# Kernel optimization log

Hardware: AMD Instinct MI355X
Metric: run time of the kernel (lower is better)

## Reference

```python
import jax, jax.numpy as jnp
import numpy as np

N_NODES = 100000
N_EDGES = 1600000
H = 64
EPS_SM = 1e-16
NEG_SLOPE = 0.01  # LeakyReLU default
BN_EPS = 1e-5


def leaky_relu(x):
    return jnp.where(x >= 0, x, NEG_SLOPE * x)


def transformer_conv(x, src, tgt, edge_attr, Wq, bq, Wk, bk, Wv, bv, We, Ws, bs):
    # PyG TransformerConv, heads=1, concat=True, root_weight=True, lin_edge bias=False
    n = x.shape[0]
    q = x @ Wq + bq            # [N,H]
    k = x @ Wk + bk            # [N,H]
    v = x @ Wv + bv            # [N,H]
    e = edge_attr @ We         # [E,H]
    ke = k[src] + e            # [E,H]
    score = jnp.sum(q[tgt] * ke, axis=-1) / jnp.sqrt(jnp.float32(H))  # [E]
    # segment softmax over incoming edges of each target node
    m = jax.ops.segment_max(score, tgt, num_segments=n)
    m = jnp.where(jnp.isfinite(m), m, 0.0)
    p = jnp.exp(score - m[tgt])
    denom = jax.ops.segment_sum(p, tgt, num_segments=n)
    alpha = p / (denom[tgt] + EPS_SM)
    msg = (v[src] + e) * alpha[:, None]                  # [E,H]
    out = jax.ops.segment_sum(msg, tgt, num_segments=n)  # [N,H]
    return out + x @ Ws + bs


def batch_norm(x, gamma, beta):
    mean = jnp.mean(x, axis=0)
    var = jnp.mean((x - mean) ** 2, axis=0)
    return (x - mean) / jnp.sqrt(var + BN_EPS) * gamma + beta


def setup_inputs() -> dict:
    key = jax.random.key(0)
    ks = jax.random.split(key, 24)
    s = 0.05
    d = {
        "x": jax.random.normal(ks[0], (N_NODES, 2), jnp.float32),
        "edge_index": jax.random.randint(ks[1], (2, N_EDGES), 0, N_NODES, jnp.int32),
        "edge_attr": jax.random.normal(ks[2], (N_EDGES, 2), jnp.float32),
        "mask": jax.random.uniform(ks[3], (N_NODES,), jnp.float32),
        # gcn1 (in=2)
        "Wq1": jax.random.normal(ks[4], (2, H)) * s, "bq1": jnp.zeros((H,)),
        "Wk1": jax.random.normal(ks[5], (2, H)) * s, "bk1": jnp.zeros((H,)),
        "Wv1": jax.random.normal(ks[6], (2, H)) * s, "bv1": jnp.zeros((H,)),
        "We1": jax.random.normal(ks[7], (2, H)) * s,
        "Ws1": jax.random.normal(ks[8], (2, H)) * s, "bs1": jnp.zeros((H,)),
        # gcn2 (in=64)
        "Wq2": jax.random.normal(ks[9], (H, H)) * s, "bq2": jnp.zeros((H,)),
        "Wk2": jax.random.normal(ks[10], (H, H)) * s, "bk2": jnp.zeros((H,)),
        "Wv2": jax.random.normal(ks[11], (H, H)) * s, "bv2": jnp.zeros((H,)),
        "We2": jax.random.normal(ks[12], (2, H)) * s,
        "Ws2": jax.random.normal(ks[13], (H, H)) * s, "bs2": jnp.zeros((H,)),
        # batch norm
        "bn_gamma": jnp.ones((H,)), "bn_beta": jnp.zeros((H,)),
        # final MLP 64->32->1
        "Wf1": jax.random.normal(ks[14], (H, 32)) * s, "bf1": jnp.zeros((32,)),
        "Wf2": jax.random.normal(ks[15], (32, 1)) * s, "bf2": jnp.zeros((1,)),
        "iterations": 3,
    }
    return d


def reference(x, edge_index, edge_attr, mask,
              Wq1, bq1, Wk1, bk1, Wv1, bv1, We1, Ws1, bs1,
              Wq2, bq2, Wk2, bk2, Wv2, bv2, We2, Ws2, bs2,
              bn_gamma, bn_beta, Wf1, bf1, Wf2, bf2, iterations):
    src, tgt = edge_index[0], edge_index[1]
    h = transformer_conv(x, src, tgt, edge_attr, Wq1, bq1, Wk1, bk1, Wv1, bv1, We1, Ws1, bs1)
    h = leaky_relu(batch_norm(h, bn_gamma, bn_beta))
    h = leaky_relu(transformer_conv(h, src, tgt, edge_attr, Wq2, bq2, Wk2, bk2, Wv2, bv2, We2, Ws2, bs2))
    for _ in range(iterations - 1):
        h = leaky_relu(transformer_conv(h, src, tgt, edge_attr, Wq2, bq2, Wk2, bk2, Wv2, bv2, We2, Ws2, bs2))
    out = jnp.squeeze(leaky_relu(h @ Wf1 + bf1) @ Wf2 + bf2, axis=-1)  # [N]
    return out * mask
```

## Files before the change

### kernel.cpp

```cpp
#include <hip/hip_runtime.h>
#include <hip/hip_fp16.h>

#define N_NODES 100000
#define N_EDGES 1600000
#define SCAN_B ((N_NODES + 1023) / 1024)
#define BSHIFT 7
#define NB_BKT ((N_NODES + 127) / 128)
#define BCAP 2560

typedef _Float16 half2_t __attribute__((ext_vector_type(2)));
typedef _Float16 half8_t __attribute__((ext_vector_type(8)));
typedef float f32x4 __attribute__((ext_vector_type(4)));

__device__ __forceinline__ float lrelu(float x) { return x >= 0.f ? x : 0.01f * x; }

__global__ void k_count(const int* __restrict__ tgt, int* __restrict__ deg) {
    int i = blockIdx.x * 256 + threadIdx.x;
    atomicAdd(&deg[tgt[i]], 1);
}

__global__ void k_scan1(const int* __restrict__ deg, int* __restrict__ bsum) {
    __shared__ int s[256];
    int t = threadIdx.x;
    int gi = blockIdx.x * 1024 + t * 4;
    int v = 0;
    if (gi < N_NODES) {
        int4 d = *(const int4*)&deg[gi];
        v = d.x + d.y + d.z + d.w;
    }
    s[t] = v;
    __syncthreads();
    for (int d = 128; d > 0; d >>= 1) {
        if (t < d) s[t] += s[t + d];
        __syncthreads();
    }
    if (t == 0) bsum[blockIdx.x] = s[0];
}

__global__ void k_scan2(int* bsum, int* rowptr) {
    if (threadIdx.x == 0) {
        int run = 0;
        for (int b = 0; b < SCAN_B; b++) {
            int v = bsum[b];
            bsum[b] = run;
            run += v;
        }
        rowptr[N_NODES] = run;
    }
}

__global__ void k_scan3(const int* __restrict__ deg, const int* __restrict__ bsum,
                        int* __restrict__ rowptr, int* __restrict__ fill) {
    __shared__ int s[256];
    int t = threadIdx.x;
    int gi = blockIdx.x * 1024 + t * 4;
    int4 d = make_int4(0, 0, 0, 0);
    if (gi < N_NODES) d = *(const int4*)&deg[gi];
    int tsum = d.x + d.y + d.z + d.w;
    s[t] = tsum;
    __syncthreads();
    for (int dd = 1; dd < 256; dd <<= 1) {
        int val = (t >= dd) ? s[t - dd] : 0;
        __syncthreads();
        s[t] += val;
        __syncthreads();
    }
    int texcl = s[t] - tsum + bsum[blockIdx.x];
    if (gi < N_NODES) {
        int4 w;
        w.x = texcl;
        w.y = texcl + d.x;
        w.z = texcl + d.x + d.y;
        w.w = texcl + d.x + d.y + d.z;
        *(int4*)&rowptr[gi] = w;
        *(int4*)&fill[gi] = w;
    }
}

__global__ void k_scatter(const int* __restrict__ src, const int* __restrict__ tgt,
                          const float2* __restrict__ ea,
                          int* __restrict__ fill, int2* __restrict__ csr) {
    int i = blockIdx.x * 256 + threadIdx.x;
    int t = tgt[i];
    float2 e = ea[i];
    int pos = atomicAdd(&fill[t], 1);
    __half2 h2 = __floats2half2_rn(e.x, e.y);
    csr[pos] = make_int2(src[i], *(int*)&h2);
}

__global__ __launch_bounds__(256) void k_bin1(const int* __restrict__ src,
                                              const int* __restrict__ tgt,
                                              const float2* __restrict__ ea,
                                              int* __restrict__ gCur,
                                              int2* __restrict__ bin) {
    __shared__ int hist[NB_BKT];
    __shared__ int cur[NB_BKT];
    int tid = threadIdx.x;
    for (int b = tid; b < NB_BKT; b += 256) hist[b] = 0;
    __syncthreads();
    int base = blockIdx.x * 6400;
#pragma unroll 5
    for (int k = 0; k < 25; k++) {
        int i = base + k * 256 + tid;
        atomicAdd(&hist[tgt[i] >> BSHIFT], 1);
    }
    __syncthreads();
    for (int b = tid; b < NB_BKT; b += 256)
        cur[b] = atomicAdd(&gCur[b], hist[b]);
    __syncthreads();
    for (int k = 0; k < 25; k++) {
        int i = base + k * 256 + tid;
        int t = tgt[i];
        int b = t >> BSHIFT;
        float2 e = ea[i];
        int pos = atomicAdd(&cur[b], 1);
        if (pos < BCAP) {
            __half2 h2 = __floats2half2_rn(e.x, e.y);
            int2 rec;
            rec.x = src[i] | ((t & 127) << 20);
            rec.y = *(int*)&h2;
            bin[(size_t)b * BCAP + pos] = rec;
        }
    }
}

__global__ __launch_bounds__(256) void k_bin2(const int* __restrict__ gCnt,
                                              const int2* __restrict__ bin,
                                              int2* __restrict__ csr,
                                              int* __restrict__ fill) {
    __shared__ int cnt[128];
    int tid = threadIdx.x;
    if (tid < 128) cnt[tid] = 0;
    __syncthreads();
    int b = blockIdx.x;
    int nb = min(gCnt[b], BCAP);
    const int2* myb = &bin[(size_t)b * BCAP];
    for (int i = tid; i < nb; i += 256) {
        int2 rec = myb[i];
        int tloc = (rec.x >> 20) & 127;
        int s = rec.x & 0xFFFFF;
        int pos = atomicAdd(&cnt[tloc], 1);
        if (pos < 64) {
            int node = (b << BSHIFT) + tloc;
            csr[((size_t)node << 6) + pos] = make_int2(s | (rec.x & 0xFFF00000), rec.y);
        }
    }
    __syncthreads();
    if (tid < 128) {
        int node = (b << BSHIFT) + tid;
        if (node < N_NODES) fill[node] = min(cnt[tid], 64);
    }
}

__global__ void k_prep2(const float* __restrict__ Wq, const float* __restrict__ Wk,
                        const float* __restrict__ Ws, const float* __restrict__ We,
                        const float* __restrict__ bk, float* __restrict__ Wcomb) {
    int idx = blockIdx.x * 256 + threadIdx.x;
    if (idx >= 9216) return;
    int j = idx / 144;
    int m = idx - j * 144;
    float v = 0.f;
    if (m < 64) {
        float s = 0.f;
        for (int ch = 0; ch < 64; ch++) s += Wq[j * 64 + ch] * Wk[m * 64 + ch];
        v = 0.125f * s;
    } else if (m < 128) {
        v = Ws[j * 64 + (m - 64)];
    } else if (m == 128) {
        float s = 0.f;
        for (int ch = 0; ch < 64; ch++) s += Wq[j * 64 + ch] * bk[ch];
        v = 0.125f * s;
    } else if (m <= 130) {
        float s = 0.f;
        for (int ch = 0; ch < 64; ch++) s += Wq[j * 64 + ch] * We[(m - 129) * 64 + ch];
        v = 0.125f * s;
    }
    Wcomb[idx] = v;
}

__global__ void k_prepb(const float* __restrict__ Wk2, const float* __restrict__ We2,
                        const float* __restrict__ bq2, const float* __restrict__ bk2,
                        const float* __restrict__ bs2, const float* __restrict__ Wq1,
                        const float* __restrict__ Wk1, const float* __restrict__ We1,
                        const float* __restrict__ bq1, const float* __restrict__ bk1,
                        float* __restrict__ bcomb) {
    int t = threadIdx.x;
    if (t >= 160) return;
    float v = 0.f;
    if (t < 64) {
        float s = 0.f;
        for (int i = 0; i < 64; i++) s += Wk2[t * 64 + i] * bq2[i];
        v = 0.125f * s;
    } else if (t < 128) {
        v = bs2[t - 64];
    } else if (t == 128) {
        float s = 0.f;
        for (int i = 0; i < 64; i++) s += bq2[i] * bk2[i];
        v = 0.125f * s;
    } else if (t <= 130) {
        float s = 0.f;
        for (int i = 0; i < 64; i++) s += bq2[i] * We2[(t - 129) * 64 + i];
        v = 0.125f * s;
    } else if (t < 144) {
        v = 0.f;
    } else {
        int t2 = t - 144;
        float s = 0.f;
        if (t2 < 4) {
            int j = t2 >> 1, m = t2 & 1;
            for (int ch = 0; ch < 64; ch++) s += Wq1[j * 64 + ch] * Wk1[m * 64 + ch];
        } else if (t2 < 6) {
            int j = t2 - 4;
            for (int ch = 0; ch < 64; ch++) s += Wq1[j * 64 + ch] * bk1[ch];
        } else if (t2 < 8) {
            int m = t2 - 6;
            for (int ch = 0; ch < 64; ch++) s += bq1[ch] * Wk1[m * 64 + ch];
        } else if (t2 == 8) {
            for (int ch = 0; ch < 64; ch++) s += bq1[ch] * bk1[ch];
        } else if (t2 < 13) {
            int j = (t2 - 9) >> 1, d = (t2 - 9) & 1;
            for (int ch = 0; ch < 64; ch++) s += Wq1[j * 64 + ch] * We1[d * 64 + ch];
        } else if (t2 < 15) {
            int d = t2 - 13;
            for (int ch = 0; ch < 64; ch++) s += bq1[ch] * We1[d * 64 + ch];
        }
        v = 0.125f * s;
    }
    bcomb[t] = v;
}

__global__ void k_prepw(const float* __restrict__ Wcomb, __half* __restrict__ wp) {
    int t = blockIdx.x * 256 + threadIdx.x;
    if (t >= 9216) return;
    int e = t & 7;
    int lane = (t >> 3) & 63;
    int kh = (t >> 9) & 1;
    int fm = t >> 10;
    int k = (kh << 5) + ((lane >> 4) << 3) + e;
    int c = fm * 16 + (lane & 15);
    wp[t] = __float2half(Wcomb[k * 144 + c]);
}

__global__ void k_prepv(const float* __restrict__ Wv, __half* __restrict__ wvp) {
    int t = blockIdx.x * 256 + threadIdx.x;
    if (t >= 4096) return;
    int e = t & 7;
    int lane = (t >> 3) & 63;
    int kh = (t >> 9) & 1;
    int fm = t >> 10;
    int k = (kh << 5) + ((lane >> 4) << 3) + e;
    int c = fm * 16 + (lane & 15);
    wvp[t] = __float2half(Wv[k * 64 + c]);
}

__global__ __launch_bounds__(256) void k_agg1(
    const float* __restrict__ x, const int* __restrict__ idx,
    const int2* __restrict__ csr, const float* __restrict__ Wv,
    const float* __restrict__ We, const float* __restrict__ Ws,
    const float* __restrict__ bv, const float* __restrict__ bs,
    const float* __restrict__ prep, __half* __restrict__ oh, int bucket) {
    int node = blockIdx.x * 4 + (threadIdx.x >> 6);
    int lane = threadIdx.x & 63;
    float2 xt = *(const float2*)&x[(size_t)node << 1];
    float a0 = xt.x * prep[0] + xt.y * prep[2] + prep[6];
    float a1 = xt.x * prep[1] + xt.y * prep[3] + prep[7];
    float b1 = xt.x * prep[4] + xt.y * prep[5] + prep[8];
    float g0 = xt.x * prep[9] + xt.y * prep[11] + prep[13];
    float g1 = xt.x * prep[10] + xt.y * prep[12] + prep[14];

    float l = 0.f, px0 = 0.f, px1 = 0.f, pA = 0.f, pB = 0.f;
    if (bucket) {
        int deg = idx[node];
        bool valid = lane < deg;
        int2 rec = valid ? csr[((size_t)node << 6) + lane] : make_int2(0, 0);
        int src = rec.x & 0xFFFFF;
        float2 ef = __half22float2(*(__half2*)&rec.y);
        float2 xs = valid ? *(const float2*)&x[(size_t)src << 1] : make_float2(0.f, 0.f);
        float t = a0 * xs.x + a1 * xs.y + b1 + g0 * ef.x + g1 * ef.y;
        float pp = valid ? __expf(t) : 0.f;
        l = pp;
        px0 = pp * xs.x;
        px1 = pp * xs.y;
        pA = pp * ef.x;
        pB = pp * ef.y;
    } else {
        int beg = idx[node], end = idx[node + 1];
        for (int p = beg + lane; p < end; p += 64) {
            int2 rec = csr[p];
            float2 ef = __half22float2(*(__half2*)&rec.y);
            float2 xs = *(const float2*)&x[(size_t)rec.x << 1];
            float t = a0 * xs.x + a1 * xs.y + b1 + g0 * ef.x + g1 * ef.y;
            float pp = __expf(t);
            l += pp;
            px0 += pp * xs.x;
            px1 += pp * xs.y;
            pA += pp * ef.x;
            pB += pp * ef.y;
        }
    }
#pragma unroll
    for (int D = 1; D < 64; D <<= 1) {
        l += __shfl_xor(l, D, 64);
        px0 += __shfl_xor(px0, D, 64);
        px1 += __shfl_xor(px1, D, 64);
        pA += __shfl_xor(pA, D, 64);
        pB += __shfl_xor(pB, D, 64);
    }
    float inv = 1.f / (l + 1e-16f);
    int c = lane;
    float r = (px0 * Wv[c] + px1 * Wv[64 + c] + pA * We[c] + pB * We[64 + c] +
               l * bv[c]) * inv +
              xt.x * Ws[c] + xt.y * Ws[64 + c] + bs[c];
    oh[((size_t)node << 6) + c] = __float2half(r);
}

__global__ void k_bnp(const __half* __restrict__ oh, float* __restrict__ bnsum,
                      float* __restrict__ bnsq) {
    __shared__ float s1[256], s2[256];
    int t = threadIdx.x;
    int c = t & 63, nsub = t >> 6;
    float su = 0.f, sq = 0.f;
    int base = blockIdx.x * 400;
    for (int i = 0; i < 100; i++) {
        int node = base + i * 4 + nsub;
        float v = __half2float(oh[((size_t)node << 6) + c]);
        su += v;
        sq += v * v;
    }
    s1[t] = su;
    s2[t] = sq;
    __syncthreads();
    if (t < 64) {
        float a = s1[t] + s1[t + 64] + s1[t + 128] + s1[t + 192];
        float b = s2[t] + s2[t + 64] + s2[t + 128] + s2[t + 192];
        atomicAdd(&bnsum[t], a);
        atomicAdd(&bnsq[t], b);
    }
}

__global__ void k_bnf(const float* bnsum, const float* bnsq, const float* gamma,
                      const float* beta, float* bnab) {
    int c = threadIdx.x;
    float mean = bnsum[c] * (1.f / N_NODES);
    float var = bnsq[c] * (1.f / N_NODES) - mean * mean;
    float A = gamma[c] * rsqrtf(var + 1e-5f);
    bnab[c] = A;
    bnab[64 + c] = beta[c] - mean * A;
}

__global__ void k_bna(const __half* __restrict__ oh, const float* __restrict__ bnab,
                      __half* __restrict__ hh) {
    int idx = blockIdx.x * 256 + threadIdx.x;
    int c = idx & 63;
    float v = lrelu(__half2float(oh[idx]) * bnab[c] + bnab[64 + c]);
    hh[idx] = __float2half(v);
}

__global__ __launch_bounds__(256) void k_gemm(
    const __half* __restrict__ oh, const __half* __restrict__ hhin,
    const __half* __restrict__ wp, const float* __restrict__ bcomb,
    const float* __restrict__ bnab, int use_bn,
    __half* __restrict__ qh, float* __restrict__ ext, __half* __restrict__ hhout) {
    __shared__ __half qsm[64 * 68];
    int tid = threadIdx.x;
    int w = tid >> 6;
    int lane = tid & 63;
    int nloc = lane & 15;
    int kg = lane >> 4;
    int base = blockIdx.x * 64;

    half8_t A[2], AE[2];
    const half8_t* wpv = (const half8_t*)wp;
#pragma unroll
    for (int kh = 0; kh < 2; kh++) A[kh] = wpv[((w << 1) + kh) * 64 + lane];
    if (w == 3) {
#pragma unroll
        for (int kh = 0; kh < 2; kh++) AE[kh] = wpv[((8 << 1) + kh) * 64 + lane];
    }

    half8_t z8;
#pragma unroll
    for (int i = 0; i < 8; i++) z8[i] = (_Float16)0.f;

    half8_t B[4][2];
    int n[4];
    bool g[4];
#pragma unroll
    for (int nf = 0; nf < 4; nf++) {
        n[nf] = base + (nf << 4) + nloc;
        g[nf] = n[nf] < N_NODES;
    }

    if (use_bn) {
        float4 bnA[2][2], bnB[2][2];
#pragma unroll
        for (int kh = 0; kh < 2; kh++) {
            int k0 = (kh << 5) + (kg << 3);
            bnA[kh][0] = *(const float4*)&bnab[k0];
            bnA[kh][1] = *(const float4*)&bnab[k0 + 4];
            bnB[kh][0] = *(const float4*)&bnab[64 + k0];
            bnB[kh][1] = *(const float4*)&bnab[64 + k0 + 4];
        }
        const int4 zi4 = make_int4(0, 0, 0, 0);
#pragma unroll
        for (int nf = 0; nf < 4; nf++) {
            const __half* orow = oh + ((size_t)n[nf] << 6);
#pragma unroll
            for (int kh = 0; kh < 2; kh++) {
                int k0 = (kh << 5) + (kg << 3);
                int4 raw = g[nf] ? *(const int4*)&orow[k0] : zi4;
                const __half2* op = (const __half2*)&raw;
                float2 o01 = __half22float2(op[0]);
                float2 o23 = __half22float2(op[1]);
                float2 o45 = __half22float2(op[2]);
                float2 o67 = __half22float2(op[3]);
                float4 lo, hi;
                lo.x = lrelu(o01.x * bnA[kh][0].x + bnB[kh][0].x);
                lo.y = lrelu(o01.y * bnA[kh][0].y + bnB[kh][0].y);
                lo.z = lrelu(o23.x * bnA[kh][0].z + bnB[kh][0].z);
                lo.w = lrelu(o23.y * bnA[kh][0].w + bnB[kh][0].w);
                hi.x = lrelu(o45.x * bnA[kh][1].x + bnB[kh][1].x);
                hi.y = lrelu(o45.y * bnA[kh][1].y + bnB[kh][1].y);
                hi.z = lrelu(o67.x * bnA[kh][1].z + bnB[kh][1].z);
                hi.w = lrelu(o67.y * bnA[kh][1].w + bnB[kh][1].w);
                half8_t r;
                r[0] = (_Float16)lo.x; r[1] = (_Float16)lo.y;
                r[2] = (_Float16)lo.z; r[3] = (_Float16)lo.w;
                r[4] = (_Float16)hi.x; r[5] = (_Float16)hi.y;
                r[6] = (_Float16)hi.z; r[7] = (_Float16)hi.w;
                B[nf][kh] = r;
                if (g[nf]) *(half8_t*)&hhout[((size_t)n[nf] << 6) + k0] = r;
            }
        }
    } else {
#pragma unroll
        for (int nf = 0; nf < 4; nf++) {
#pragma unroll
            for (int kh = 0; kh < 2; kh++) {
                int k0 = (kh << 5) + (kg << 3);
                B[nf][kh] = g[nf] ? *(const half8_t*)&hhin[((size_t)n[nf] << 6) + k0]
                                  : z8;
            }
        }
    }

    f32x4 acc[4], accE[4];
#pragma unroll
    for (int nf = 0; nf < 4; nf++) {
        acc[nf] = (f32x4){0.f, 0.f, 0.f, 0.f};
        accE[nf] = (f32x4){0.f, 0.f, 0.f, 0.f};
    }

#pragma unroll
    for (int nf = 0; nf < 4; nf++) {
        acc[nf] = __builtin_amdgcn_mfma_f32_16x16x32_f16(A[0], B[nf][0], acc[nf],
                                                          0, 0, 0);
        acc[nf] = __builtin_amdgcn_mfma_f32_16x16x32_f16(A[1], B[nf][1], acc[nf],
                                                          0, 0, 0);
    }
    if (w == 3) {
#pragma unroll
        for (int nf = 0; nf < 4; nf++) {
            accE[nf] = __builtin_amdgcn_mfma_f32_16x16x32_f16(AE[0], B[nf][0],
                                                              accE[nf], 0, 0, 0);
            accE[nf] = __builtin_amdgcn_mfma_f32_16x16x32_f16(AE[1], B[nf][1],
                                                              accE[nf], 0, 0, 0);
        }
    }

    int rowg = kg << 2;
    int c0 = (w << 4) + rowg;
    float4 bi = *(const float4*)&bcomb[c0];
#pragma unroll
    for (int nf = 0; nf < 4; nf++) {
        int nl = (nf << 4) + nloc;
        __half2 p0 = __floats2half2_rn(acc[nf][0] + bi.x, acc[nf][1] + bi.y);
        __half2 p1 = __floats2half2_rn(acc[nf][2] + bi.z, acc[nf][3] + bi.w);
        *(__half2*)&qsm[nl * 68 + c0] = p0;
        *(__half2*)&qsm[nl * 68 + c0 + 2] = p1;
    }
    if (w == 3 && kg == 0) {
        float4 be = *(const float4*)&bcomb[128];
#pragma unroll
        for (int nf = 0; nf < 4; nf++) {
            if (!g[nf]) continue;
            float4 r;
            r.x = accE[nf][0] + be.x;
            r.y = accE[nf][1] + be.y;
            r.z = accE[nf][2] + be.z;
            r.w = accE[nf][3] + be.w;
            *(float4*)&ext[(size_t)n[nf] << 2] = r;
        }
    }
    __syncthreads();
#pragma unroll
    for (int rep = 0; rep < 8; rep++) {
        int i = rep * 256 + tid;
        int row = i >> 5;
        int col = (i & 31) << 1;
        if (base + row < N_NODES) {
            int v = *(int*)&qsm[row * 68 + col];
            *(int*)&qh[((size_t)(base + row) << 6) + col] = v;
        }
    }
}

template <int LAST>
__global__ __launch_bounds__(256) void k_fused(
    __half* qh, float* ext,
    const __half* __restrict__ hh_in, __half* __restrict__ hh_out,
    const int* __restrict__ idx, const int2* __restrict__ csr,
    const __half* __restrict__ wp, const __half* __restrict__ wvp,
    const float* __restrict__ We, const float* __restrict__ bv,
    const float* __restrict__ bcomb,
    const float* __restrict__ Wf1, const float* __restrict__ bf1,
    const float* __restrict__ Wf2, const float* __restrict__ bf2v,
    const float* __restrict__ mask, float* __restrict__ out,
    int bucket) {
    constexpr int RSM_BYTES = LAST ? (64 * 68 * 4) : (64 * 72 * 2);
    __shared__ __align__(16) char smem[RSM_BYTES + 9216 + 1024];
    __half* rsm16 = (__half*)smem;
    float* rsm32 = (float*)smem;
    __half* Shatsm = (__half*)(smem + RSM_BYTES);
    __half* qsm = (__half*)(smem + RSM_BYTES);
    float* W1sm = (float*)(smem + RSM_BYTES);
    float4* svecsm = (float4*)(smem + RSM_BYTES + 9216);

    int tid = threadIdx.x;
    int wv = tid >> 6;
    int lane = tid & 63;
    int base = blockIdx.x * 64;

    {
        int es = lane >> 2, cl = lane & 3;
        int jf = ((es & 1) << 3) | ((es & 2) << 1) | ((es & 4) >> 1) | ((es & 8) >> 3);
        int shatcol = (cl << 4) + jf;
        for (int nl = 0; nl < 16; nl++) {
            int node = base + (wv << 4) + nl;
            if (node >= N_NODES) continue;
            float4 ex = *(const float4*)&ext[(size_t)node << 2];
            float beta = ex.x, qe0 = ex.y, qe1 = ex.z;
            int4 qr0 = *(const int4*)&qh[((size_t)node << 6) + (cl << 4)];
            int4 qr1 = *(const int4*)&qh[((size_t)node << 6) + (cl << 4) + 8];
            const half2_t* qp0 = (const half2_t*)&qr0;
            const half2_t* qp1 = (const half2_t*)&qr1;

            float l = 0.f, sA = 0.f, sB = 0.f;
            float accv[16];
#pragma unroll
            for (int c = 0; c < 16; c++) accv[c] = 0.f;

            int nEdge, rbase2;
            if (bucket) {
                nEdge = idx[node];
                rbase2 = node << 6;
            } else {
                rbase2 = idx[node];
                nEdge = idx[node + 1] - rbase2;
            }
            int nIter = (nEdge + 15) >> 4;

            auto body = [&](int4 h0, int4 h1, int2 rec, bool ok) {
                const half2_t* hp0 = (const half2_t*)&h0;
                const half2_t* hp1 = (const half2_t*)&h1;
                float t = 0.f;
#if __has_builtin(__builtin_amdgcn_fdot2)
#pragma unroll
                for (int p = 0; p < 4; p++)
                    t = __builtin_amdgcn_fdot2(hp0[p], qp0[p], t, false);
#pragma unroll
                for (int p = 0; p < 4; p++)
                    t = __builtin_amdgcn_fdot2(hp1[p], qp1[p], t, false);
#else
                const __half* hq0 = (const __half*)&qr0;
                const __half* hq1 = (const __half*)&qr1;
                const __half* hh0 = (const __half*)&h0;
                const __half* hh1 = (const __half*)&h1;
#pragma unroll
                for (int c = 0; c < 8; c++)
                    t += __half2float(hh0[c]) * __half2float(hq0[c]);
#pragma unroll
                for (int c = 0; c < 8; c++)
                    t += __half2float(hh1[c]) * __half2float(hq1[c]);
#endif
                t += __shfl_xor(t, 1, 64);
                t += __shfl_xor(t, 2, 64);
                float2 ef = __half22float2(*(__half2*)&rec.y);
                t += beta + ef.x * qe0 + ef.y * qe1;
                float pp = ok ? __expf(t) : 0.f;
                l += pp;
                sA += pp * ef.x;
                sB += pp * ef.y;
                const __half* hs0 = (const __half*)&h0;
                const __half* hs1 = (const __half*)&h1;
#pragma unroll
                for (int c = 0; c < 8; c++) accv[c] += pp * __half2float(hs0[c]);
#pragma unroll
                for (int c = 0; c < 8; c++) accv[8 + c] += pp * __half2float(hs1[c]);
            };

            if (bucket) {
                int2 recs[4];
#pragma unroll
                for (int i = 0; i < 4; i++) {
                    int e = (i << 4) + es;
                    recs[i] = (e < nEdge) ? csr[(size_t)rbase2 + e] : make_int2(0, 0);
                }
                if (nIter > 0) {
                    int src0 = recs[0].x & 0xFFFFF;
                    const __half* hr = hh_in + ((size_t)src0 << 6) + (cl << 4);
                    int4 h0c = *(const int4*)&hr[0];
                    int4 h1c = *(const int4*)&hr[8];
#pragma unroll
                    for (int i = 0; i < 4; i++) {
                        if (i < nIter) {
                            int4 h0 = h0c, h1 = h1c;
                            if (i + 1 < nIter) {
                                int srcn = recs[i + 1].x & 0xFFFFF;
                                const __half* hrn =
                                    hh_in + ((size_t)srcn << 6) + (cl << 4);
                                h0c = *(const int4*)&hrn[0];
                                h1c = *(const int4*)&hrn[8];
                            }
                            body(h0, h1, recs[i], ((i << 4) + es) < nEdge);
                        }
                    }
                }
            } else {
                for (int i = 0; i < nIter; i++) {
                    int e = (i << 4) + es;
                    bool ok = e < nEdge;
                    int2 rec = ok ? csr[(size_t)rbase2 + e] : make_int2(0, 0);
                    int src = rec.x & 0xFFFFF;
                    const __half* hr = hh_in + ((size_t)src << 6) + (cl << 4);
                    int4 h0 = *(const int4*)&hr[0];
                    int4 h1 = *(const int4*)&hr[8];
                    body(h0, h1, rec, ok);
                }
            }

#pragma unroll
            for (int D = 4; D < 64; D <<= 1) {
                l += __shfl_xor(l, D, 64);
                sA += __shfl_xor(sA, D, 64);
                sB += __shfl_xor(sB, D, 64);
            }
            float inv = 1.f / (l + 1e-16f);

#pragma unroll
            for (int step = 0; step < 4; step++) {
                int m = 4 << step;
                int half = 8 >> step;
                bool up = (lane & m) != 0;
#pragma unroll
                for (int i = 0; i < half; i++) {
                    float send = up ? accv[i] : accv[i + half];
                    float recv = __shfl_xor(send, m, 64);
                    float keep = up ? accv[i + half] : accv[i];
                    accv[i] = keep + recv;
                }
            }
            Shatsm[((wv << 4) + nl) * 72 + shatcol] = __float2half(accv[0] * inv);
            if (lane == 0)
                svecsm[(wv << 4) + nl] = make_float4(sA * inv, sB * inv, l * inv, 0.f);
        }
    }
    __syncthreads();

    {
        int nloc = lane & 15, kg = lane >> 4;
        const half8_t* wvv = (const half8_t*)wvp;
        const half8_t* wpv = (const half8_t*)wp;
        half8_t Av0 = wvv[((wv << 1) + 0) * 64 + lane];
        half8_t Av1 = wvv[((wv << 1) + 1) * 64 + lane];
        half8_t As0 = wpv[(((4 + wv) << 1) + 0) * 64 + lane];
        half8_t As1 = wpv[(((4 + wv) << 1) + 1) * 64 + lane];

        int rowg = kg << 2;
        int c0 = (wv << 4) + rowg;
        float4 we0 = *(const float4*)&We[c0];
        float4 we1 = *(const float4*)&We[64 + c0];
        float4 bv4 = *(const float4*)&bv[c0];
        float4 bs4 = *(const float4*)&bcomb[64 + c0];

        half8_t z8;
#pragma unroll
        for (int i = 0; i < 8; i++) z8[i] = (_Float16)0.f;

#pragma unroll
        for (int nf = 0; nf < 4; nf++) {
            int n = base + (nf << 4) + nloc;
            bool g = n < N_NODES;
            int nl2 = (nf << 4) + nloc;
            const __half* srow = &Shatsm[nl2 * 72];
            const __half* hrow = hh_in + ((size_t)n << 6);
            half8_t Bs0 = g ? *(const half8_t*)&srow[kg << 3] : z8;
            half8_t Bs1 = g ? *(const half8_t*)&srow[32 + (kg << 3)] : z8;
            half8_t Bh0 = g ? *(const half8_t*)&hrow[kg << 3] : z8;
            half8_t Bh1 = g ? *(const half8_t*)&hrow[32 + (kg << 3)] : z8;

            f32x4 acc = (f32x4){0.f, 0.f, 0.f, 0.f};
            acc = __builtin_amdgcn_mfma_f32_16x16x32_f16(Av0, Bs0, acc, 0, 0, 0);
            acc = __builtin_amdgcn_mfma_f32_16x16x32_f16(Av1, Bs1, acc, 0, 0, 0);
            acc = __builtin_amdgcn_mfma_f32_16x16x32_f16(As0, Bh0, acc, 0, 0, 0);
            acc = __builtin_amdgcn_mfma_f32_16x16x32_f16(As1, Bh1, acc, 0, 0, 0);

            float4 sv = g ? svecsm[nl2] : make_float4(0.f, 0.f, 0.f, 0.f);
            float4 r;
            r.x = lrelu(acc[0] + sv.x * we0.x + sv.y * we1.x + sv.z * bv4.x + bs4.x);
            r.y = lrelu(acc[1] + sv.x * we0.y + sv.y * we1.y + sv.z * bv4.y + bs4.y);
            r.z = lrelu(acc[2] + sv.x * we0.z + sv.y * we1.z + sv.z * bv4.z + bs4.z);
            r.w = lrelu(acc[3] + sv.x * we0.w + sv.y * we1.w + sv.z * bv4.w + bs4.w);

            if (LAST) {
                *(float4*)&rsm32[nl2 * 68 + c0] = r;
            } else {
                __half2 p0 = __floats2half2_rn(r.x, r.y);
                __half2 p1 = __floats2half2_rn(r.z, r.w);
                *(__half2*)&rsm16[nl2 * 72 + c0] = p0;
                *(__half2*)&rsm16[nl2 * 72 + c0 + 2] = p1;
            }
        }
    }
    __syncthreads();

    if (!LAST) {
        int nloc = lane & 15, kg = lane >> 4;
        const half8_t* wpv = (const half8_t*)wp;
        half8_t A0 = wpv[((wv << 1) + 0) * 64 + lane];
        half8_t A1 = wpv[((wv << 1) + 1) * 64 + lane];
        half8_t AE0 = A0, AE1 = A1;
        if (wv == 3) {
            AE0 = wpv[16 * 64 + lane];
            AE1 = wpv[17 * 64 + lane];
        }
        int rowg = kg << 2;
        int c0 = (wv << 4) + rowg;
        float4 bi = *(const float4*)&bcomb[c0];

#pragma unroll
        for (int nf = 0; nf < 4; nf++) {
            int nl2 = (nf << 4) + nloc;
            const __half* rrow = &rsm16[nl2 * 72];
            half8_t B0 = *(const half8_t*)&rrow[kg << 3];
            half8_t B1 = *(const half8_t*)&rrow[32 + (kg << 3)];
            f32x4 acc = (f32x4){0.f, 0.f, 0.f, 0.f};
            acc = __builtin_amdgcn_mfma_f32_16x16x32_f16(A0, B0, acc, 0, 0, 0);
            acc = __builtin_amdgcn_mfma_f32_16x16x32_f16(A1, B1, acc, 0, 0, 0);
            __half2 p0 = __floats2half2_rn(acc[0] + bi.x, acc[1] + bi.y);
            __half2 p1 = __floats2half2_rn(acc[2] + bi.z, acc[3] + bi.w);
            *(__half2*)&qsm[nl2 * 72 + c0] = p0;
            *(__half2*)&qsm[nl2 * 72 + c0 + 2] = p1;
            if (wv == 3) {
                f32x4 ae = (f32x4){0.f, 0.f, 0.f, 0.f};
                ae = __builtin_amdgcn_mfma_f32_16x16x32_f16(AE0, B0, ae, 0, 0, 0);
                ae = __builtin_amdgcn_mfma_f32_16x16x32_f16(AE1, B1, ae, 0, 0, 0);
                if (kg == 0) {
                    int n = base + nl2;
                    if (n < N_NODES) {
                        float4 be = *(const float4*)&bcomb[128];
                        float4 r;
                        r.x = ae[0] + be.x;
                        r.y = ae[1] + be.y;
                        r.z = ae[2] + be.z;
                        r.w = ae[3] + be.w;
                        *(float4*)&ext[(size_t)n << 2] = r;
                    }
                }
            }
        }
        __syncthreads();
#pragma unroll
        for (int rep = 0; rep < 8; rep++) {
            int i = rep * 256 + tid;
            int row = i >> 5;
            int col = (i & 31) << 1;
            if (base + row < N_NODES) {
                *(int*)&qh[((size_t)(base + row) << 6) + col] =
                    *(int*)&qsm[row * 72 + col];
                *(int*)&hh_out[((size_t)(base + row) << 6) + col] =
                    *(int*)&rsm16[row * 72 + col];
            }
        }
    } else {
        for (int i = tid; i < 2048; i += 256) W1sm[i] = Wf1[i];
        __syncthreads();
        int nl2 = tid >> 2, jg = tid & 3;
        int node = base + nl2;
        float a8[8];
        const float* b1p = &bf1[jg << 3];
#pragma unroll
        for (int k = 0; k < 8; k++) a8[k] = b1p[k];
        const float* hr = &rsm32[nl2 * 68];
        for (int c = 0; c < 64; c++) {
            float hv = hr[c];
            const float* wr = &W1sm[(c << 5) + (jg << 3)];
            float4 wa = *(const float4*)&wr[0];
            float4 wb = *(const float4*)&wr[4];
            a8[0] += hv * wa.x; a8[1] += hv * wa.y;
            a8[2] += hv * wa.z; a8[3] += hv * wa.w;
            a8[4] += hv * wb.x; a8[5] += hv * wb.y;
            a8[6] += hv * wb.z; a8[7] += hv * wb.w;
        }
        const float* w2p = &Wf2[jg << 3];
        float zs = 0.f;
#pragma unroll
        for (int k = 0; k < 8; k++) zs += lrelu(a8[k]) * w2p[k];
        zs += __shfl_xor(zs, 1, 64);
        zs += __shfl_xor(zs, 2, 64);
        if (jg == 0 && node < N_NODES)
            out[node] = (zs + bf2v[0]) * mask[node];
    }
}

extern "C" void kernel_launch(void* const* d_in, const int* in_sizes, int n_in,
                              void* d_out, int out_size, void* d_ws, size_t ws_size,
                              hipStream_t stream) {
    const float* x = (const float*)d_in[0];
    const int* ei = (const int*)d_in[1];
    const float* ea = (const float*)d_in[2];
    const float* mask = (const float*)d_in[3];
    const float *Wq1 = (const float*)d_in[4], *bq1 = (const float*)d_in[5];
    const float *Wk1 = (const float*)d_in[6], *bk1 = (const float*)d_in[7];
    const float *Wv1 = (const float*)d_in[8], *bv1 = (const float*)d_in[9];
    const float *We1 = (const float*)d_in[10];
    const float *Ws1 = (const float*)d_in[11], *bs1 = (const float*)d_in[12];
    const float *Wq2 = (const float*)d_in[13], *bq2 = (const float*)d_in[14];
    const float *Wk2 = (const float*)d_in[15], *bk2 = (const float*)d_in[16];
    const float *Wv2 = (const float*)d_in[17], *bv2 = (const float*)d_in[18];
    const float *We2 = (const float*)d_in[19];
    const float *Ws2 = (const float*)d_in[20], *bs2 = (const float*)d_in[21];
    const float *gamma = (const float*)d_in[22], *beta = (const float*)d_in[23];
    const float *Wf1 = (const float*)d_in[24], *bf1 = (const float*)d_in[25];
    const float *Wf2 = (const float*)d_in[26], *bf2v = (const float*)d_in[27];
    float* out = (float*)d_out;

    const size_t bucket_need =
        (size_t)NB_BKT * BCAP * 8 + (size_t)N_NODES * 64 * 8 +
        (size_t)N_NODES * 64 * 2 * 4 +
        (size_t)N_NODES * 16 +
        (size_t)N_NODES * 4 * 3 + (1 << 20);
    bool use_bucket = ws_size >= bucket_need;

    char* ws = (char*)d_ws;
    size_t off = 0;
    auto alloc = [&](size_t b) {
        size_t r = off;
        off += (b + 255) & ~(size_t)255;
        return r;
    };
    int* deg = (int*)(ws + alloc(N_NODES * 4));
    int* fill = (int*)(ws + alloc(N_NODES * 4));
    int* rowptr = (int*)(ws + alloc((N_NODES + 1) * 4));
    int* bsum = (int*)(ws + alloc(SCAN_B * 4));
    int* gCur = (int*)(ws + alloc(NB_BKT * 4));
    float* bnsum = (float*)(ws + alloc(64 * 4));
    float* bnsq = (float*)(ws + alloc(64 * 4));
    float* bnab = (float*)(ws + alloc(128 * 4));
    float* Wcomb = (float*)(ws + alloc(9216 * 4));
    float* bcomb = (float*)(ws + alloc(160 * 4));
    __half* wp = (__half*)(ws + alloc(9216 * 2));
    __half* wvp = (__half*)(ws + alloc(4096 * 2));
    float* ext = (float*)(ws + alloc((size_t)N_NODES * 16));
    int2* bin1 = (int2*)(ws + alloc(use_bucket ? (size_t)NB_BKT * BCAP * 8 : 256));
    int2* csr = (int2*)(ws + alloc(use_bucket ? (size_t)N_NODES * 64 * 8
                                              : (size_t)N_EDGES * 8));
    __half* qh = (__half*)(ws + alloc((size_t)N_NODES * 64 * 2));
    __half* oh = (__half*)(ws + alloc((size_t)N_NODES * 64 * 2));
    __half* hh0 = (__half*)(ws + alloc((size_t)N_NODES * 64 * 2));
    __half* hh1 = (__half*)(ws + alloc((size_t)N_NODES * 64 * 2));

    const int* srcI = ei;
    const int* tgtI = ei + N_EDGES;

    hipMemsetAsync(bnsum, 0, 64 * 4, stream);
    hipMemsetAsync(bnsq, 0, 64 * 4, stream);

    k_prep2<<<36, 256, 0, stream>>>(Wq2, Wk2, Ws2, We2, bk2, Wcomb);
    k_prepb<<<1, 192, 0, stream>>>(Wk2, We2, bq2, bk2, bs2, Wq1, Wk1, We1, bq1, bk1,
                                   bcomb);
    k_prepw<<<36, 256, 0, stream>>>(Wcomb, wp);
    k_prepv<<<16, 256, 0, stream>>>(Wv2, wvp);

    const int* aggIdx;
    if (use_bucket) {
        hipMemsetAsync(gCur, 0, NB_BKT * 4, stream);
        k_bin1<<<250, 256, 0, stream>>>(srcI, tgtI, (const float2*)ea, gCur, bin1);
        k_bin2<<<NB_BKT, 256, 0, stream>>>(gCur, bin1, csr, fill);
        aggIdx = fill;
    } else {
        hipMemsetAsync(deg, 0, N_NODES * 4, stream);
        k_count<<<N_EDGES / 256, 256, 0, stream>>>(tgtI, deg);
        k_scan1<<<SCAN_B, 256, 0, stream>>>(deg, bsum);
        k_scan2<<<1, 64, 0, stream>>>(bsum, rowptr);
        k_scan3<<<SCAN_B, 256, 0, stream>>>(deg, bsum, rowptr, fill);
        k_scatter<<<N_EDGES / 256, 256, 0, stream>>>(srcI, tgtI, (const float2*)ea,
                                                     fill, csr);
        aggIdx = rowptr;
    }
    int bkt = use_bucket ? 1 : 0;

    k_agg1<<<N_NODES / 4, 256, 0, stream>>>(x, aggIdx, csr, Wv1, We1, Ws1, bv1, bs1,
                                            bcomb + 144, oh, bkt);
    k_bnp<<<250, 256, 0, stream>>>(oh, bnsum, bnsq);
    k_bnf<<<1, 64, 0, stream>>>(bnsum, bnsq, gamma, beta, bnab);
    if (!use_bucket)
        k_bna<<<N_NODES * 64 / 256, 256, 0, stream>>>(oh, bnab, hh0);

    const int gemm_grid = (N_NODES + 63) / 64;
    k_gemm<<<gemm_grid, 256, 0, stream>>>(oh, hh0, wp, bcomb, bnab, bkt, qh, ext,
                                          hh0);
    k_fused<0><<<gemm_grid, 256, 0, stream>>>(qh, ext, hh0, hh1, aggIdx, csr, wp,
                                              wvp, We2, bv2, bcomb, Wf1, bf1, Wf2,
                                              bf2v, mask, out, bkt);
    k_fused<0><<<gemm_grid, 256, 0, stream>>>(qh, ext, hh1, hh0, aggIdx, csr, wp,
                                              wvp, We2, bv2, bcomb, Wf1, bf1, Wf2,
                                              bf2v, mask, out, bkt);
    k_fused<1><<<gemm_grid, 256, 0, stream>>>(qh, ext, hh0, hh1, aggIdx, csr, wp,
                                              wvp, We2, bv2, bcomb, Wf1, bf1, Wf2,
                                              bf2v, mask, out, bkt);
}
```

Before: 531.9 us.

## Fuse BN stats into agg1 and first-layer GEMM into fused conv kernel

BatchNorm partial sums are now computed in k_agg1's epilogue and spread over 32 atomic slots, removing the separate k_bnp pass over the activations. The standalone k_gemm is removed. The first k_fused instance now computes q and the edge-projection terms for its own 64-node tile with MFMA into shared memory, avoiding a global write and re-read of qh and ext. k_bna is now always launched to materialise the normalized activations, which replaces the BN application previously folded into k_gemm. Other blocks' q/ext still come from global memory for later layers, so correctness relies on the later fused kernels reading qh/ext written by this first one.

```diff
diff --git a/kernel.cpp b/kernel.cpp
--- a/kernel.cpp
+++ b/kernel.cpp
@@ -258,9 +258,12 @@
     const int2* __restrict__ csr, const float* __restrict__ Wv,
     const float* __restrict__ We, const float* __restrict__ Ws,
     const float* __restrict__ bv, const float* __restrict__ bs,
-    const float* __restrict__ prep, __half* __restrict__ oh, int bucket) {
-    int node = blockIdx.x * 4 + (threadIdx.x >> 6);
-    int lane = threadIdx.x & 63;
+    const float* __restrict__ prep, __half* __restrict__ oh,
+    float* __restrict__ bnsum, float* __restrict__ bnsq, int bucket) {
+    __shared__ float s1[256], s2[256];
+    int tid = threadIdx.x;
+    int node = blockIdx.x * 4 + (tid >> 6);
+    int lane = tid & 63;
     float2 xt = *(const float2*)&x[(size_t)node << 1];
     float a0 = xt.x * prep[0] + xt.y * prep[2] + prep[6];
     float a1 = xt.x * prep[1] + xt.y * prep[3] + prep[7];
@@ -312,37 +315,28 @@
                l * bv[c]) * inv +
               xt.x * Ws[c] + xt.y * Ws[64 + c] + bs[c];
     oh[((size_t)node << 6) + c] = __float2half(r);
-}
-
-__global__ void k_bnp(const __half* __restrict__ oh, float* __restrict__ bnsum,
-                      float* __restrict__ bnsq) {
-    __shared__ float s1[256], s2[256];
-    int t = threadIdx.x;
-    int c = t & 63, nsub = t >> 6;
-    float su = 0.f, sq = 0.f;
-    int base = blockIdx.x * 400;
-    for (int i = 0; i < 100; i++) {
-        int node = base + i * 4 + nsub;
-        float v = __half2float(oh[((size_t)node << 6) + c]);
-        su += v;
-        sq += v * v;
-    }
-    s1[t] = su;
-    s2[t] = sq;
-    __syncthreads();
-    if (t < 64) {
-        float a = s1[t] + s1[t + 64] + s1[t + 128] + s1[t + 192];
-        float b = s2[t] + s2[t + 64] + s2[t + 128] + s2[t + 192];
-        atomicAdd(&bnsum[t], a);
-        atomicAdd(&bnsq[t], b);
+    s1[tid] = r;
+    s2[tid] = r * r;
+    __syncthreads();
+    if (tid < 64) {
+        float a = s1[tid] + s1[tid + 64] + s1[tid + 128] + s1[tid + 192];
+        float b = s2[tid] + s2[tid + 64] + s2[tid + 128] + s2[tid + 192];
+        int slot = (blockIdx.x & 31) << 6;
+        atomicAdd(&bnsum[slot + tid], a);
+        atomicAdd(&bnsq[slot + tid], b);
     }
 }
 
 __global__ void k_bnf(const float* bnsum, const float* bnsq, const float* gamma,
                       const float* beta, float* bnab) {
     int c = threadIdx.x;
-    float mean = bnsum[c] * (1.f / N_NODES);
-    float var = bnsq[c] * (1.f / N_NODES) - mean * mean;
+    float su = 0.f, sq = 0.f;
+    for (int s = 0; s < 32; s++) {
+        su += bnsum[(s << 6) + c];
+        sq += bnsq[(s << 6) + c];
+    }
+    float mean = su * (1.f / N_NODES);
+    float var = sq * (1.f / N_NODES) - mean * mean;
     float A = gamma[c] * rsqrtf(var + 1e-5f);
     bnab[c] = A;
     bnab[64 + c] = beta[c] - mean * A;
@@ -356,156 +350,7 @@
     hh[idx] = __float2half(v);
 }
 
-__global__ __launch_bounds__(256) void k_gemm(
-    const __half* __restrict__ oh, const __half* __restrict__ hhin,
-    const __half* __restrict__ wp, const float* __restrict__ bcomb,
-    const float* __restrict__ bnab, int use_bn,
-    __half* __restrict__ qh, float* __restrict__ ext, __half* __restrict__ hhout) {
-    __shared__ __half qsm[64 * 68];
-    int tid = threadIdx.x;
-    int w = tid >> 6;
-    int lane = tid & 63;
-    int nloc = lane & 15;
-    int kg = lane >> 4;
-    int base = blockIdx.x * 64;
-
-    half8_t A[2], AE[2];
-    const half8_t* wpv = (const half8_t*)wp;
-#pragma unroll
-    for (int kh = 0; kh < 2; kh++) A[kh] = wpv[((w << 1) + kh) * 64 + lane];
-    if (w == 3) {
-#pragma unroll
-        for (int kh = 0; kh < 2; kh++) AE[kh] = wpv[((8 << 1) + kh) * 64 + lane];
-    }
-
-    half8_t z8;
-#pragma unroll
-    for (int i = 0; i < 8; i++) z8[i] = (_Float16)0.f;
-
-    half8_t B[4][2];
-    int n[4];
-    bool g[4];
-#pragma unroll
-    for (int nf = 0; nf < 4; nf++) {
-        n[nf] = base + (nf << 4) + nloc;
-        g[nf] = n[nf] < N_NODES;
-    }
-
-    if (use_bn) {
-        float4 bnA[2][2], bnB[2][2];
-#pragma unroll
-        for (int kh = 0; kh < 2; kh++) {
-            int k0 = (kh << 5) + (kg << 3);
-            bnA[kh][0] = *(const float4*)&bnab[k0];
-            bnA[kh][1] = *(const float4*)&bnab[k0 + 4];
-            bnB[kh][0] = *(const float4*)&bnab[64 + k0];
-            bnB[kh][1] = *(const float4*)&bnab[64 + k0 + 4];
-        }
-        const int4 zi4 = make_int4(0, 0, 0, 0);
-#pragma unroll
-        for (int nf = 0; nf < 4; nf++) {
-            const __half* orow = oh + ((size_t)n[nf] << 6);
-#pragma unroll
-            for (int kh = 0; kh < 2; kh++) {
-                int k0 = (kh << 5) + (kg << 3);
-                int4 raw = g[nf] ? *(const int4*)&orow[k0] : zi4;
-                const __half2* op = (const __half2*)&raw;
-                float2 o01 = __half22float2(op[0]);
-                float2 o23 = __half22float2(op[1]);
-                float2 o45 = __half22float2(op[2]);
-                float2 o67 = __half22float2(op[3]);
-                float4 lo, hi;
-                lo.x = lrelu(o01.x * bnA[kh][0].x + bnB[kh][0].x);
-                lo.y = lrelu(o01.y * bnA[kh][0].y + bnB[kh][0].y);
-                lo.z = lrelu(o23.x * bnA[kh][0].z + bnB[kh][0].z);
-                lo.w = lrelu(o23.y * bnA[kh][0].w + bnB[kh][0].w);
-                hi.x = lrelu(o45.x * bnA[kh][1].x + bnB[kh][1].x);
-                hi.y = lrelu(o45.y * bnA[kh][1].y + bnB[kh][1].y);
-                hi.z = lrelu(o67.x * bnA[kh][1].z + bnB[kh][1].z);
-                hi.w = lrelu(o67.y * bnA[kh][1].w + bnB[kh][1].w);
-                half8_t r;
-                r[0] = (_Float16)lo.x; r[1] = (_Float16)lo.y;
-                r[2] = (_Float16)lo.z; r[3] = (_Float16)lo.w;
-                r[4] = (_Float16)hi.x; r[5] = (_Float16)hi.y;
-                r[6] = (_Float16)hi.z; r[7] = (_Float16)hi.w;
-                B[nf][kh] = r;
-                if (g[nf]) *(half8_t*)&hhout[((size_t)n[nf] << 6) + k0] = r;
-            }
-        }
-    } else {
-#pragma unroll
-        for (int nf = 0; nf < 4; nf++) {
-#pragma unroll
-            for (int kh = 0; kh < 2; kh++) {
-                int k0 = (kh << 5) + (kg << 3);
-                B[nf][kh] = g[nf] ? *(const half8_t*)&hhin[((size_t)n[nf] << 6) + k0]
-                                  : z8;
-            }
-        }
-    }
-
-    f32x4 acc[4], accE[4];
-#pragma unroll
-    for (int nf = 0; nf < 4; nf++) {
-        acc[nf] = (f32x4){0.f, 0.f, 0.f, 0.f};
-        accE[nf] = (f32x4){0.f, 0.f, 0.f, 0.f};
-    }
-
-#pragma unroll
-    for (int nf = 0; nf < 4; nf++) {
-        acc[nf] = __builtin_amdgcn_mfma_f32_16x16x32_f16(A[0], B[nf][0], acc[nf],
-                                                          0, 0, 0);
-        acc[nf] = __builtin_amdgcn_mfma_f32_16x16x32_f16(A[1], B[nf][1], acc[nf],
-                                                          0, 0, 0);
-    }
-    if (w == 3) {
-#pragma unroll
-        for (int nf = 0; nf < 4; nf++) {
-            accE[nf] = __builtin_amdgcn_mfma_f32_16x16x32_f16(AE[0], B[nf][0],
-                                                              accE[nf], 0, 0, 0);
-            accE[nf] = __builtin_amdgcn_mfma_f32_16x16x32_f16(AE[1], B[nf][1],
-                                                              accE[nf], 0, 0, 0);
-        }
-    }
-
-    int rowg = kg << 2;
-    int c0 = (w << 4) + rowg;
-    float4 bi = *(const float4*)&bcomb[c0];
-#pragma unroll
-    for (int nf = 0; nf < 4; nf++) {
-        int nl = (nf << 4) + nloc;
-        __half2 p0 = __floats2half2_rn(acc[nf][0] + bi.x, acc[nf][1] + bi.y);
-        __half2 p1 = __floats2half2_rn(acc[nf][2] + bi.z, acc[nf][3] + bi.w);
-        *(__half2*)&qsm[nl * 68 + c0] = p0;
-        *(__half2*)&qsm[nl * 68 + c0 + 2] = p1;
-    }
-    if (w == 3 && kg == 0) {
-        float4 be = *(const float4*)&bcomb[128];
-#pragma unroll
-        for (int nf = 0; nf < 4; nf++) {
-            if (!g[nf]) continue;
-            float4 r;
-            r.x = accE[nf][0] + be.x;
-            r.y = accE[nf][1] + be.y;
-            r.z = accE[nf][2] + be.z;
-            r.w = accE[nf][3] + be.w;
-            *(float4*)&ext[(size_t)n[nf] << 2] = r;
-        }
-    }
-    __syncthreads();
-#pragma unroll
-    for (int rep = 0; rep < 8; rep++) {
-        int i = rep * 256 + tid;
-        int row = i >> 5;
-        int col = (i & 31) << 1;
-        if (base + row < N_NODES) {
-            int v = *(int*)&qsm[row * 68 + col];
-            *(int*)&qh[((size_t)(base + row) << 6) + col] = v;
-        }
-    }
-}
-
-template <int LAST>
+template <int FIRST, int LAST>
 __global__ __launch_bounds__(256) void k_fused(
     __half* qh, float* ext,
     const __half* __restrict__ hh_in, __half* __restrict__ hh_out,
@@ -518,18 +363,66 @@
     const float* __restrict__ mask, float* __restrict__ out,
     int bucket) {
     constexpr int RSM_BYTES = LAST ? (64 * 68 * 4) : (64 * 72 * 2);
-    __shared__ __align__(16) char smem[RSM_BYTES + 9216 + 1024];
+    constexpr int EXT_BYTES = FIRST ? 1024 : 0;
+    __shared__ __align__(16) char smem[RSM_BYTES + 9216 + 1024 + EXT_BYTES];
     __half* rsm16 = (__half*)smem;
     float* rsm32 = (float*)smem;
+    __half* qsmA = (__half*)smem;
     __half* Shatsm = (__half*)(smem + RSM_BYTES);
     __half* qsm = (__half*)(smem + RSM_BYTES);
     float* W1sm = (float*)(smem + RSM_BYTES);
     float4* svecsm = (float4*)(smem + RSM_BYTES + 9216);
+    float4* extsm = (float4*)(smem + RSM_BYTES + 9216 + 1024);
 
     int tid = threadIdx.x;
     int wv = tid >> 6;
     int lane = tid & 63;
     int base = blockIdx.x * 64;
+
+    if (FIRST) {
+        int nloc = lane & 15, kg = lane >> 4;
+        const half8_t* wpv = (const half8_t*)wp;
+        half8_t A0 = wpv[((wv << 1) + 0) * 64 + lane];
+        half8_t A1 = wpv[((wv << 1) + 1) * 64 + lane];
+        half8_t AE0 = A0, AE1 = A1;
+        if (wv == 3) {
+            AE0 = wpv[16 * 64 + lane];
+            AE1 = wpv[17 * 64 + lane];
+        }
+        int rowg = kg << 2;
+        int c0 = (wv << 4) + rowg;
+        float4 bi = *(const float4*)&bcomb[c0];
+        half8_t z8;
+#pragma unroll
+        for (int i = 0; i < 8; i++) z8[i] = (_Float16)0.f;
+#pragma unroll
+        for (int nf = 0; nf < 4; nf++) {
+            int n = base + (nf << 4) + nloc;
+            bool g = n < N_NODES;
+            int nl2 = (nf << 4) + nloc;
+            const __half* hrow = hh_in + ((size_t)n << 6);
+            half8_t B0 = g ? *(const half8_t*)&hrow[kg << 3] : z8;
+            half8_t B1 = g ? *(const half8_t*)&hrow[32 + (kg << 3)] : z8;
+            f32x4 acc = (f32x4){0.f, 0.f, 0.f, 0.f};
+            acc = __builtin_amdgcn_mfma_f32_16x16x32_f16(A0, B0, acc, 0, 0, 0);
+            acc = __builtin_amdgcn_mfma_f32_16x16x32_f16(A1, B1, acc, 0, 0, 0);
+            __half2 p0 = __floats2half2_rn(acc[0] + bi.x, acc[1] + bi.y);
+            __half2 p1 = __floats2half2_rn(acc[2] + bi.z, acc[3] + bi.w);
+            *(__half2*)&qsmA[nl2 * 72 + c0] = p0;
+            *(__half2*)&qsmA[nl2 * 72 + c0 + 2] = p1;
+            if (wv == 3) {
+                f32x4 ae = (f32x4){0.f, 0.f, 0.f, 0.f};
+                ae = __builtin_amdgcn_mfma_f32_16x16x32_f16(AE0, B0, ae, 0, 0, 0);
+                ae = __builtin_amdgcn_mfma_f32_16x16x32_f16(AE1, B1, ae, 0, 0, 0);
+                if (kg == 0 && g) {
+                    float4 be = *(const float4*)&bcomb[128];
+                    extsm[nl2] = make_float4(ae[0] + be.x, ae[1] + be.y,
+                                             ae[2] + be.z, ae[3] + be.w);
+                }
+            }
+        }
+        __syncthreads();
+    }
 
     {
         int es = lane >> 2, cl = lane & 3;
@@ -538,10 +431,18 @@
         for (int nl = 0; nl < 16; nl++) {
             int node = base + (wv << 4) + nl;
             if (node >= N_NODES) continue;
-            float4 ex = *(const float4*)&ext[(size_t)node << 2];
+            float4 ex;
+            int4 qr0, qr1;
+            if (FIRST) {
+                ex = extsm[(wv << 4) + nl];
+                qr0 = *(const int4*)&qsmA[((wv << 4) + nl) * 72 + (cl << 4)];
+                qr1 = *(const int4*)&qsmA[((wv << 4) + nl) * 72 + (cl << 4) + 8];
+            } else {
+                ex = *(const float4*)&ext[(size_t)node << 2];
+                qr0 = *(const int4*)&qh[((size_t)node << 6) + (cl << 4)];
+                qr1 = *(const int4*)&qh[((size_t)node << 6) + (cl << 4) + 8];
+            }
             float beta = ex.x, qe0 = ex.y, qe1 = ex.z;
-            int4 qr0 = *(const int4*)&qh[((size_t)node << 6) + (cl << 4)];
-            int4 qr1 = *(const int4*)&qh[((size_t)node << 6) + (cl << 4) + 8];
             const half2_t* qp0 = (const half2_t*)&qr0;
             const half2_t* qp1 = (const half2_t*)&qr1;
 
@@ -854,8 +755,8 @@
     int* rowptr = (int*)(ws + alloc((N_NODES + 1) * 4));
     int* bsum = (int*)(ws + alloc(SCAN_B * 4));
     int* gCur = (int*)(ws + alloc(NB_BKT * 4));
-    float* bnsum = (float*)(ws + alloc(64 * 4));
-    float* bnsq = (float*)(ws + alloc(64 * 4));
+    float* bnsum = (float*)(ws + alloc(32 * 64 * 4));
+    float* bnsq = (float*)(ws + alloc(32 * 64 * 4));
     float* bnab = (float*)(ws + alloc(128 * 4));
     float* Wcomb = (float*)(ws + alloc(9216 * 4));
     float* bcomb = (float*)(ws + alloc(160 * 4));
@@ -873,8 +774,8 @@
     const int* srcI = ei;
     const int* tgtI = ei + N_EDGES;
 
-    hipMemsetAsync(bnsum, 0, 64 * 4, stream);
-    hipMemsetAsync(bnsq, 0, 64 * 4, stream);
+    hipMemsetAsync(bnsum, 0, 32 * 64 * 4, stream);
+    hipMemsetAsync(bnsq, 0, 32 * 64 * 4, stream);
 
     k_prep2<<<36, 256, 0, stream>>>(Wq2, Wk2, Ws2, We2, bk2, Wcomb);
     k_prepb<<<1, 192, 0, stream>>>(Wk2, We2, bq2, bk2, bs2, Wq1, Wk1, We1, bq1, bk1,
@@ -901,22 +802,18 @@
     int bkt = use_bucket ? 1 : 0;
 
     k_agg1<<<N_NODES / 4, 256, 0, stream>>>(x, aggIdx, csr, Wv1, We1, Ws1, bv1, bs1,
-                                            bcomb + 144, oh, bkt);
-    k_bnp<<<250, 256, 0, stream>>>(oh, bnsum, bnsq);
+                                            bcomb + 144, oh, bnsum, bnsq, bkt);
     k_bnf<<<1, 64, 0, stream>>>(bnsum, bnsq, gamma, beta, bnab);
-    if (!use_bucket)
-        k_bna<<<N_NODES * 64 / 256, 256, 0, stream>>>(oh, bnab, hh0);
+    k_bna<<<N_NODES * 64 / 256, 256, 0, stream>>>(oh, bnab, hh0);
 
     const int gemm_grid = (N_NODES + 63) / 64;
-    k_gemm<<<gemm_grid, 256, 0, stream>>>(oh, hh0, wp, bcomb, bnab, bkt, qh, ext,
-                                          hh0);
-    k_fused<0><<<gemm_grid, 256, 0, stream>>>(qh, ext, hh0, hh1, aggIdx, csr, wp,
-                                              wvp, We2, bv2, bcomb, Wf1, bf1, Wf2,
-                                              bf2v, mask, out, bkt);
-    k_fused<0><<<gemm_grid, 256, 0, stream>>>(qh, ext, hh1, hh0, aggIdx, csr, wp,
-                                              wvp, We2, bv2, bcomb, Wf1, bf1, Wf2,
-                                              bf2v, mask, out, bkt);
-    k_fused<1><<<gemm_grid, 256, 0, stream>>>(qh, ext, hh0, hh1, aggIdx, csr, wp,
-                                              wvp, We2, bv2, bcomb, Wf1, bf1, Wf2,
-                                              bf2v, mask, out, bkt);
-}
+    k_fused<1, 0><<<gemm_grid, 256, 0, stream>>>(qh, ext, hh0, hh1, aggIdx, csr, wp,
+                                                 wvp, We2, bv2, bcomb, Wf1, bf1, Wf2,
+                                                 bf2v, mask, out, bkt);
+    k_fused<0, 0><<<gemm_grid, 256, 0, stream>>>(qh, ext, hh1, hh0, aggIdx, csr, wp,
+                                                 wvp, We2, bv2, bcomb, Wf1, bf1, Wf2,
+                                                 bf2v, mask, out, bkt);
+    k_fused<0, 1><<<gemm_grid, 256, 0, stream>>>(qh, ext, hh0, hh1, aggIdx, csr, wp,
+                                                 wvp, We2, bv2, bcomb, Wf1, bf1, Wf2,
+                                                 bf2v, mask, out, bkt);
+}
```

New measurement: 504.9 us. 5.1% less time.
